# Kernel tuning notes

Hardware: AMD Instinct MI355X
Metric: run time of the kernel (lower is better)

## Reference

```python
import jax, jax.numpy as jnp
import numpy as np

COST_CLASS, COST_BBOX, COST_GIOU = 1.0, 5.0, 2.0

def box_cxcywh_to_xyxy(b):
    cx, cy, w, h = b[..., 0], b[..., 1], b[..., 2], b[..., 3]
    return jnp.stack([cx - 0.5 * w, cy - 0.5 * h, cx + 0.5 * w, cy + 0.5 * h], axis=-1)

def generalized_box_iou(b1, b2):
    # b1: [bs, Q, 4] xyxy, b2: [bs, T, 4] xyxy -> [bs, Q, T]
    area1 = (b1[..., 2] - b1[..., 0]) * (b1[..., 3] - b1[..., 1])  # [bs,Q]
    area2 = (b2[..., 2] - b2[..., 0]) * (b2[..., 3] - b2[..., 1])  # [bs,T]
    b1e = b1[:, :, None, :]  # [bs,Q,1,4]
    b2e = b2[:, None, :, :]  # [bs,1,T,4]
    lt = jnp.maximum(b1e[..., :2], b2e[..., :2])
    rb = jnp.minimum(b1e[..., 2:], b2e[..., 2:])
    wh = jnp.clip(rb - lt, 0.0)
    inter = wh[..., 0] * wh[..., 1]                       # [bs,Q,T]
    union = area1[:, :, None] + area2[:, None, :] - inter
    iou = inter / union
    # smallest enclosing box
    lt_e = jnp.minimum(b1e[..., :2], b2e[..., :2])
    rb_e = jnp.maximum(b1e[..., 2:], b2e[..., 2:])
    wh_e = jnp.clip(rb_e - lt_e, 0.0)
    area_e = wh_e[..., 0] * wh_e[..., 1]
    return iou - (area_e - union) / area_e

def setup_inputs() -> dict:
    key = jax.random.key(0)
    k1, k2, k3, k4 = jax.random.split(key, 4)
    bs, Q, T, C = 256, 300, 100, 92
    return {
        "pred_logits": jax.random.normal(k1, (bs, Q, C), dtype=jnp.float32),
        "pred_boxes": jax.random.uniform(k2, (bs, Q, 4), dtype=jnp.float32),
        "tgt_labels": jax.random.randint(k3, (bs, T), 0, C),
        "tgt_boxes": jax.random.uniform(k4, (bs, T, 4), dtype=jnp.float32),
    }

def reference(pred_logits, pred_boxes, tgt_labels, tgt_boxes):
    # cost_class: -softmax(logits)[b, q, tgt_labels[b, t]]
    out_prob = jax.nn.softmax(pred_logits, axis=-1)                      # [bs,Q,C]
    cost_class = -jnp.take_along_axis(out_prob, tgt_labels[:, None, :], axis=2)  # [bs,Q,T]
    # cost_bbox: pairwise L1 distance between box coords
    cost_bbox = jnp.sum(jnp.abs(pred_boxes[:, :, None, :] - tgt_boxes[:, None, :, :]), axis=-1)
    # cost_giou: negative generalized IoU in xyxy coords
    cost_giou = -generalized_box_iou(box_cxcywh_to_xyxy(pred_boxes), box_cxcywh_to_xyxy(tgt_boxes))
    C = COST_BBOX * cost_bbox + COST_CLASS * cost_class + COST_GIOU * cost_giou  # [bs,Q,T]
    return C
```

## Files before the change

### kernel.cpp

```cpp
#include <hip/hip_runtime.h>

constexpr int BS = 256;
constexpr int NQ = 300;
constexpr int NT = 100;
constexpr int NC = 92;
constexpr int QT = 60;
constexpr int NTILES = NQ / QT;
constexpr int BLOCK = 256;
constexpr int PSTRIDE = 93;

__device__ __forceinline__ float rcpf(float x) { return __builtin_amdgcn_rcpf(x); }

__global__ __launch_bounds__(BLOCK) void matcher_kernel(
    const float* __restrict__ logits,
    const float* __restrict__ pboxes,
    const int*   __restrict__ tlabels,
    const float* __restrict__ tboxes,
    float* __restrict__ out)
{
    __shared__ float  prob[QT * PSTRIDE];
    __shared__ float4 t_xy[NT];
    __shared__ int    t_lab[NT];
    __shared__ float4 p_xy[QT];

    const int b    = blockIdx.x / NTILES;
    const int q0   = (blockIdx.x % NTILES) * QT;
    const int tid  = threadIdx.x;
    const int lane = tid & 63;
    const int wave = tid >> 6;

    if (tid < NT) {
        const float4 tb = *(const float4*)(tboxes + ((size_t)b * NT + tid) * 4);
        t_xy[tid] = make_float4(tb.x - 0.5f * tb.z, tb.y - 0.5f * tb.w,
                                tb.x + 0.5f * tb.z, tb.y + 0.5f * tb.w);
        t_lab[tid] = tlabels[(size_t)b * NT + tid];
    } else if (tid >= 128 && tid < 128 + QT) {
        const int q = tid - 128;
        const float4 pb = *(const float4*)(pboxes + ((size_t)b * NQ + q0 + q) * 4);
        p_xy[q] = make_float4(pb.x - 0.5f * pb.z, pb.y - 0.5f * pb.w,
                              pb.x + 0.5f * pb.z, pb.y + 0.5f * pb.w);
    }

    const float* lbase = logits + ((size_t)b * NQ + q0) * NC;
    const int rsub = lane >> 4;
    const int c0   = lane & 15;
    for (int g = wave; g < QT / 4; g += 4) {
        const int q = g * 4 + rsub;
        const float* lr = lbase + (size_t)q * NC;
        float e[6];
        float s = 0.0f;
        #pragma unroll
        for (int k = 0; k < 6; ++k) {
            const int c = c0 + 16 * k;
            e[k] = (c < NC) ? __expf(lr[c]) : 0.0f;
            s += e[k];
        }
        s += __shfl_xor(s, 1);
        s += __shfl_xor(s, 2);
        s += __shfl_xor(s, 4);
        s += __shfl_xor(s, 8);
        const float rs = rcpf(s);
        #pragma unroll
        for (int k = 0; k < 6; ++k) {
            const int c = c0 + 16 * k;
            if (c < NC) prob[q * PSTRIDE + c] = e[k] * rs;
        }
    }
    __syncthreads();

    float* otile = out + ((size_t)b * NQ + q0) * NT;
    for (int idx = tid; idx < (QT / 2) * NT; idx += BLOCK) {
        const int q = idx / NT;
        const int t = idx - q * NT;

        const float4 tb = t_xy[t];
        const int   lab = t_lab[t];
        const float tar = (tb.z - tb.x) * (tb.w - tb.y);

        #pragma unroll
        for (int h = 0; h < 2; ++h) {
            const int qq = q + h * (QT / 2);
            const float4 p  = p_xy[qq];
            const float par = (p.z - p.x) * (p.w - p.y);
            const float plab = prob[qq * PSTRIDE + lab];

            const float ax0 = p.x - tb.x, ax1 = p.z - tb.z;
            const float ay0 = p.y - tb.y, ay1 = p.w - tb.w;
            const float bb = fmaf(0.5f, fabsf(ax0 + ax1), fabsf(ax1 - ax0))
                           + fmaf(0.5f, fabsf(ay0 + ay1), fabsf(ay1 - ay0));

            const float iw = fmaxf(fminf(p.z, tb.z) - fmaxf(p.x, tb.x), 0.0f);
            const float ih = fmaxf(fminf(p.w, tb.w) - fmaxf(p.y, tb.y), 0.0f);
            const float inter = iw * ih;
            const float uni = par + tar - inter;
            const float iou = inter * rcpf(uni);
            const float ew = fmaxf(p.z, tb.z) - fminf(p.x, tb.x);
            const float eh = fmaxf(p.w, tb.w) - fminf(p.y, tb.y);
            const float ea = ew * eh;
            const float k = (ea - uni) * rcpf(ea);

            otile[qq * NT + t] = fmaf(2.0f, k - iou, fmaf(5.0f, bb, -plab));
        }
    }
}

extern "C" void kernel_launch(void* const* d_in, const int* in_sizes, int n_in,
                              void* d_out, int out_size, void* d_ws, size_t ws_size,
                              hipStream_t stream) {
    const float* logits  = (const float*)d_in[0];
    const float* pboxes  = (const float*)d_in[1];
    const int*   tlabels = (const int*)d_in[2];
    const float* tboxes  = (const float*)d_in[3];
    float* out = (float*)d_out;
    matcher_kernel<<<dim3(BS * NTILES), dim3(BLOCK), 0, stream>>>(
        logits, pboxes, tlabels, tboxes, out);
}
```

Baseline: 22.30 us.

## Vectorize softmax logits loads with float4 and shrink query tile to 20

Logits rows (92 floats, 16-byte aligned since 92*4 is a multiple of 16) are now read and written to shared memory as float4, using 23 vectors per row. This cuts the number of scalar global loads and LDS stores. The query tile drops from 60 to 20, giving 3840 blocks instead of 1280 for better occupancy and latency hiding. The cost is that per-block setup of target boxes and labels is repeated three times as often, and waves are used less efficiently because QT/4=5 row groups are spread over 4 waves.

```diff
diff --git a/kernel.cpp b/kernel.cpp
--- a/kernel.cpp
+++ b/kernel.cpp
@@ -4,10 +4,10 @@
 constexpr int NQ = 300;
 constexpr int NT = 100;
 constexpr int NC = 92;
-constexpr int QT = 60;
+constexpr int QT = 20;
 constexpr int NTILES = NQ / QT;
 constexpr int BLOCK = 256;
-constexpr int PSTRIDE = 93;
+constexpr int PS4 = 24;
 
 __device__ __forceinline__ float rcpf(float x) { return __builtin_amdgcn_rcpf(x); }
 
@@ -18,10 +18,11 @@
     const float* __restrict__ tboxes,
     float* __restrict__ out)
 {
-    __shared__ float  prob[QT * PSTRIDE];
+    __shared__ float4 prob4[QT * PS4];
     __shared__ float4 t_xy[NT];
     __shared__ int    t_lab[NT];
     __shared__ float4 p_xy[QT];
+    float* prob = (float*)prob4;
 
     const int b    = blockIdx.x / NTILES;
     const int q0   = (blockIdx.x % NTILES) * QT;
@@ -43,28 +44,30 @@
 
     const float* lbase = logits + ((size_t)b * NQ + q0) * NC;
     const int rsub = lane >> 4;
-    const int c0   = lane & 15;
+    const int c4   = lane & 15;
     for (int g = wave; g < QT / 4; g += 4) {
         const int q = g * 4 + rsub;
-        const float* lr = lbase + (size_t)q * NC;
-        float e[6];
-        float s = 0.0f;
-        #pragma unroll
-        for (int k = 0; k < 6; ++k) {
-            const int c = c0 + 16 * k;
-            e[k] = (c < NC) ? __expf(lr[c]) : 0.0f;
-            s += e[k];
+        const float4* lr = (const float4*)(lbase + (size_t)q * NC);
+        const float4 v0 = lr[c4];
+        float4 e0, e1;
+        e0.x = __expf(v0.x); e0.y = __expf(v0.y);
+        e0.z = __expf(v0.z); e0.w = __expf(v0.w);
+        float s = e0.x + e0.y + e0.z + e0.w;
+        const bool has2 = (c4 < 23 - 16);
+        if (has2) {
+            const float4 v1 = lr[c4 + 16];
+            e1.x = __expf(v1.x); e1.y = __expf(v1.y);
+            e1.z = __expf(v1.z); e1.w = __expf(v1.w);
+            s += e1.x + e1.y + e1.z + e1.w;
         }
         s += __shfl_xor(s, 1);
         s += __shfl_xor(s, 2);
         s += __shfl_xor(s, 4);
         s += __shfl_xor(s, 8);
         const float rs = rcpf(s);
-        #pragma unroll
-        for (int k = 0; k < 6; ++k) {
-            const int c = c0 + 16 * k;
-            if (c < NC) prob[q * PSTRIDE + c] = e[k] * rs;
-        }
+        prob4[q * PS4 + c4] = make_float4(e0.x * rs, e0.y * rs, e0.z * rs, e0.w * rs);
+        if (has2)
+            prob4[q * PS4 + c4 + 16] = make_float4(e1.x * rs, e1.y * rs, e1.z * rs, e1.w * rs);
     }
     __syncthreads();
 
@@ -82,7 +85,7 @@
             const int qq = q + h * (QT / 2);
             const float4 p  = p_xy[qq];
             const float par = (p.z - p.x) * (p.w - p.y);
-            const float plab = prob[qq * PSTRIDE + lab];
+            const float plab = prob[qq * (PS4 * 4) + lab];
 
             const float ax0 = p.x - tb.x, ax1 = p.z - tb.z;
             const float ay0 = p.y - tb.y, ay1 = p.w - tb.w;
```

Measured after the change: 23.60 us. +5.8%, slower.

## Map lanes to queries, keep pred box in registers, write float4 outputs

Applied to the files above, without the earlier changes.

Restructures the pairwise phase so each lane owns one query (pred box held in registers) and each wave handles four targets at a time, writing a float4 of outputs per lane instead of scalar stores. It also simplifies the math, using cxcywh directly for the L1 term and deriving the enclosing box from the widths minus the overlap, and drops the per-element division and modulo indexing. The cost is that lanes 60-63 of each wave do redundant work and skip their stores. Each lane's float4 stores go to a different output row, so stores are strided by the row pitch rather than contiguous across lanes.

```diff
diff --git a/kernel.cpp b/kernel.cpp
--- a/kernel.cpp
+++ b/kernel.cpp
@@ -8,6 +8,7 @@
 constexpr int NTILES = NQ / QT;
 constexpr int BLOCK = 256;
 constexpr int PSTRIDE = 93;
+constexpr int PROWS = 64;
 
 __device__ __forceinline__ float rcpf(float x) { return __builtin_amdgcn_rcpf(x); }
 
@@ -18,10 +19,9 @@
     const float* __restrict__ tboxes,
     float* __restrict__ out)
 {
-    __shared__ float  prob[QT * PSTRIDE];
-    __shared__ float4 t_xy[NT];
-    __shared__ int    t_lab[NT];
-    __shared__ float4 p_xy[QT];
+    __shared__ float  prob[PROWS * PSTRIDE];
+    __shared__ float4 t_box[NT];
+    __shared__ int4   t_lab4[NT / 4];
 
     const int b    = blockIdx.x / NTILES;
     const int q0   = (blockIdx.x % NTILES) * QT;
@@ -29,16 +29,16 @@
     const int lane = tid & 63;
     const int wave = tid >> 6;
 
+    const int qg = q0 + ((lane < QT) ? lane : (QT - 1));
+    const float4 pb = *(const float4*)(pboxes + ((size_t)b * NQ + qg) * 4);
+    const float pw = pb.z, ph = pb.w;
+    const float px0 = pb.x - 0.5f * pw, py0 = pb.y - 0.5f * ph;
+    const float px1 = pb.x + 0.5f * pw, py1 = pb.y + 0.5f * ph;
+    const float par = pw * ph;
+
     if (tid < NT) {
-        const float4 tb = *(const float4*)(tboxes + ((size_t)b * NT + tid) * 4);
-        t_xy[tid] = make_float4(tb.x - 0.5f * tb.z, tb.y - 0.5f * tb.w,
-                                tb.x + 0.5f * tb.z, tb.y + 0.5f * tb.w);
-        t_lab[tid] = tlabels[(size_t)b * NT + tid];
-    } else if (tid >= 128 && tid < 128 + QT) {
-        const int q = tid - 128;
-        const float4 pb = *(const float4*)(pboxes + ((size_t)b * NQ + q0 + q) * 4);
-        p_xy[q] = make_float4(pb.x - 0.5f * pb.z, pb.y - 0.5f * pb.w,
-                              pb.x + 0.5f * pb.z, pb.y + 0.5f * pb.w);
+        t_box[tid] = *(const float4*)(tboxes + ((size_t)b * NT + tid) * 4);
+        ((int*)t_lab4)[tid] = tlabels[(size_t)b * NT + tid];
     }
 
     const float* lbase = logits + ((size_t)b * NQ + q0) * NC;
@@ -47,18 +47,15 @@
     for (int g = wave; g < QT / 4; g += 4) {
         const int q = g * 4 + rsub;
         const float* lr = lbase + (size_t)q * NC;
-        float e[6];
-        float s = 0.0f;
+        float e[6]; float s = 0.0f;
         #pragma unroll
         for (int k = 0; k < 6; ++k) {
             const int c = c0 + 16 * k;
             e[k] = (c < NC) ? __expf(lr[c]) : 0.0f;
             s += e[k];
         }
-        s += __shfl_xor(s, 1);
-        s += __shfl_xor(s, 2);
-        s += __shfl_xor(s, 4);
-        s += __shfl_xor(s, 8);
+        s += __shfl_xor(s, 1); s += __shfl_xor(s, 2);
+        s += __shfl_xor(s, 4); s += __shfl_xor(s, 8);
         const float rs = rcpf(s);
         #pragma unroll
         for (int k = 0; k < 6; ++k) {
@@ -68,39 +65,38 @@
     }
     __syncthreads();
 
-    float* otile = out + ((size_t)b * NQ + q0) * NT;
-    for (int idx = tid; idx < (QT / 2) * NT; idx += BLOCK) {
-        const int q = idx / NT;
-        const int t = idx - q * NT;
+    const float* probrow = prob + lane * PSTRIDE;
+    float* orow = out + ((size_t)b * NQ + q0 + lane) * NT;
 
-        const float4 tb = t_xy[t];
-        const int   lab = t_lab[t];
-        const float tar = (tb.z - tb.x) * (tb.w - tb.y);
+    for (int k = wave; k < NT / 4; k += 4) {
+        const int4 lb = t_lab4[k];
+        float4 res;
+        float* rp = (float*)&res;
+        const int labs[4] = {lb.x, lb.y, lb.z, lb.w};
+        #pragma unroll
+        for (int u = 0; u < 4; ++u) {
+            const float4 tb = t_box[4 * k + u];
+            const float tw = tb.z, th = tb.w;
+            const float tx0 = tb.x - 0.5f * tw, ty0 = tb.y - 0.5f * th;
+            const float tx1 = tb.x + 0.5f * tw, ty1 = tb.y + 0.5f * th;
+            const float tar = tw * th;
+            const float pl  = probrow[labs[u]];
 
-        #pragma unroll
-        for (int h = 0; h < 2; ++h) {
-            const int qq = q + h * (QT / 2);
-            const float4 p  = p_xy[qq];
-            const float par = (p.z - p.x) * (p.w - p.y);
-            const float plab = prob[qq * PSTRIDE + lab];
-
-            const float ax0 = p.x - tb.x, ax1 = p.z - tb.z;
-            const float ay0 = p.y - tb.y, ay1 = p.w - tb.w;
-            const float bb = fmaf(0.5f, fabsf(ax0 + ax1), fabsf(ax1 - ax0))
-                           + fmaf(0.5f, fabsf(ay0 + ay1), fabsf(ay1 - ay0));
-
-            const float iw = fmaxf(fminf(p.z, tb.z) - fmaxf(p.x, tb.x), 0.0f);
-            const float ih = fmaxf(fminf(p.w, tb.w) - fmaxf(p.y, tb.y), 0.0f);
+            const float bb = (fabsf(pb.x - tb.x) + fabsf(pb.y - tb.y))
+                           + (fabsf(pw - tw) + fabsf(ph - th));
+            const float dx = fminf(px1, tx1) - fmaxf(px0, tx0);
+            const float dy = fminf(py1, ty1) - fmaxf(py0, ty0);
+            const float iw = fmaxf(dx, 0.0f), ih = fmaxf(dy, 0.0f);
             const float inter = iw * ih;
-            const float uni = par + tar - inter;
+            const float uni = (par + tar) - inter;
+            const float ew = (pw + tw) - dx;
+            const float eh = (ph + th) - dy;
+            const float ea = ew * eh;
             const float iou = inter * rcpf(uni);
-            const float ew = fmaxf(p.z, tb.z) - fminf(p.x, tb.x);
-            const float eh = fmaxf(p.w, tb.w) - fminf(p.y, tb.y);
-            const float ea = ew * eh;
-            const float k = (ea - uni) * rcpf(ea);
-
-            otile[qq * NT + t] = fmaf(2.0f, k - iou, fmaf(5.0f, bb, -plab));
+            const float ur  = uni * rcpf(ea);
+            rp[u] = fmaf(-2.0f, ur, fmaf(-2.0f, iou, fmaf(5.0f, bb, 2.0f - pl)));
         }
+        if (lane < QT) *(float4*)(orow + 4 * k) = res;
     }
 }
 
```

After: 21.43 us. -3.9%, faster.
